# Optimization experiments

Hardware: AMD Instinct MI355X
Metric: run time of the kernel (lower is better)

The kernel has to match this reference:

```python
import jax, jax.numpy as jnp
import numpy as np

N = 2048      # nodes
E = 65536     # edges (avg degree 32)
NV = 6        # n_views (edge_attr dim)
C1, C2, C3 = 32, 32, 32


def _nnconv(x, edge_index, edge_attr, W, b, root, bias, in_c, out_c):
    # Edge MLP: Linear(n_views, in*out) + ReLU -> per-edge weight matrix [E, in, out]
    w = jax.nn.relu(edge_attr @ W + b).reshape(-1, in_c, out_c)
    src, dst = edge_index[0], edge_index[1]  # source_to_target flow
    msg = jnp.einsum('ei,eio->eo', x[src], w)          # gather + edge-specific matmul
    summed = jax.ops.segment_sum(msg, dst, num_segments=N)
    cnt = jax.ops.segment_sum(jnp.ones((msg.shape[0],), x.dtype), dst, num_segments=N)
    agg = summed / jnp.maximum(cnt, 1.0)[:, None]       # scatter-mean (0 for isolated nodes)
    return agg + x @ root + bias                        # root weight + bias (PyG NNConv defaults)


def setup_inputs() -> dict:
    key = jax.random.key(0)
    ks = jax.random.split(key, 12)
    s = 0.1
    return {
        'x': jax.random.normal(ks[0], (N, 1), jnp.float32),
        'edge_attr': jax.random.uniform(ks[1], (E, NV), jnp.float32),
        'edge_index': jax.random.randint(ks[2], (2, E), 0, N, jnp.int64),
        'W1': jax.random.normal(ks[3], (NV, 1 * C1), jnp.float32) * s,
        'b1': jnp.zeros((1 * C1,), jnp.float32),
        'root1': jax.random.normal(ks[4], (1, C1), jnp.float32) * s,
        'bias1': jnp.zeros((C1,), jnp.float32),
        'W2': jax.random.normal(ks[5], (NV, C1 * C2), jnp.float32) * s,
        'b2': jnp.zeros((C1 * C2,), jnp.float32),
        'root2': jax.random.normal(ks[6], (C1, C2), jnp.float32) * s,
        'bias2': jnp.zeros((C2,), jnp.float32),
        'W3': jax.random.normal(ks[7], (NV, C2 * C3), jnp.float32) * s,
        'b3': jnp.zeros((C2 * C3,), jnp.float32),
        'root3': jax.random.normal(ks[8], (C2, C3), jnp.float32) * s,
        'bias3': jnp.zeros((C3,), jnp.float32),
    }


def reference(x, edge_attr, edge_index, W1, b1, root1, bias1, W2, b2, root2, bias2, W3, b3, root3, bias3):
    h = jax.nn.relu(_nnconv(x, edge_index, edge_attr, W1, b1, root1, bias1, 1, C1))
    h = jax.nn.relu(_nnconv(h, edge_index, edge_attr, W2, b2, root2, bias2, C1, C2))
    h = jax.nn.relu(_nnconv(h, edge_index, edge_attr, W3, b3, root3, bias3, C2, C3))
    # CBT: cbt[i, j] = sum_k |h[j, k] - h[i, k]|  (all-pairs L1 distance, [N, N])
    cbt = jnp.sum(jnp.abs(h[None, :, :] - h[:, None, :]), axis=2)
    return cbt
```

## Files before the change

### kernel.cpp

```cpp
#include <hip/hip_runtime.h>

#define N_NODES 2048
#define N_EDGES 65536
#define NV 6
#define C 32


__global__ void edge1_kernel(const float* __restrict__ x,
                             const float* __restrict__ ea,
                             const int* __restrict__ src,
                             const int* __restrict__ dst,
                             const float* __restrict__ W1,
                             const float* __restrict__ b1,
                             float* __restrict__ sum1,
                             float* __restrict__ cnt) {
    int t = blockIdx.x * blockDim.x + threadIdx.x;
    int e = t >> 5, o = t & 31;
    if (e >= N_EDGES) return;
    const float* eap = ea + e * NV;
    float w = b1[o];
#pragma unroll
    for (int v = 0; v < NV; v++) w += eap[v] * W1[v * C + o];
    w = fmaxf(w, 0.0f);
    int d = dst[e];
    atomicAdd(&sum1[d * C + o], x[src[e]] * w);
    if (o == 0) atomicAdd(&cnt[d], 1.0f);
}

template <int IN_C>
__global__ void node_kernel(const float* __restrict__ sum,
                            const float* __restrict__ cnt,
                            const float* __restrict__ hprev,
                            const float* __restrict__ root,
                            const float* __restrict__ bias,
                            float* __restrict__ hout) {
    int t = blockIdx.x * blockDim.x + threadIdx.x;
    int n = t >> 5, o = t & 31;
    float inv = 1.0f / fmaxf(cnt[n], 1.0f);
    float acc = sum[t] * inv + bias[o];
#pragma unroll
    for (int i = 0; i < IN_C; i++) acc += hprev[n * IN_C + i] * root[i * C + o];
    hout[t] = fmaxf(acc, 0.0f);
}

__global__ __launch_bounds__(256) void edge23_kernel(
    const float* __restrict__ hprev,
    const float* __restrict__ ea,
    const int* __restrict__ src,
    const int* __restrict__ dst,
    const float* __restrict__ W,
    const float* __restrict__ b,
    float* __restrict__ sumout)
{
    __shared__ float Wall[7 * 1024];
    __shared__ float hb[4][32 * 4];
    for (int i = threadIdx.x; i < 6 * 1024; i += 256) Wall[i] = W[i];
    for (int i = threadIdx.x; i < 1024; i += 256) Wall[6 * 1024 + i] = b[i];
    __syncthreads();

    const int lane = threadIdx.x & 63;
    const int o = lane & 31;
    const int i0 = (lane >> 5) * 16;
    const int w = threadIdx.x >> 6;
    const int wid = (blockIdx.x * 256 + threadIdx.x) >> 6;
    const int nwaves = (gridDim.x * 256) >> 6;
    float* hbw = &hb[w][0];

    for (int g = wid; g < N_EDGES / 4; g += nwaves) {
        const int e0 = g * 4;
        int s0 = src[e0 + 0], s1 = src[e0 + 1], s2 = src[e0 + 2], s3 = src[e0 + 3];
        int d0 = dst[e0 + 0], d1 = dst[e0 + 1], d2 = dst[e0 + 2], d3 = dst[e0 + 3];
        const float* eap = ea + (size_t)e0 * NV;
        float ea0[NV], ea1[NV], ea2[NV], ea3[NV];
#pragma unroll
        for (int v = 0; v < NV; v++) {
            ea0[v] = eap[v];
            ea1[v] = eap[NV + v];
            ea2[v] = eap[2 * NV + v];
            ea3[v] = eap[3 * NV + v];
        }
        float hv0 = hprev[s0 * C + o];
        float hv1 = hprev[s1 * C + o];
        float hv2 = hprev[s2 * C + o];
        float hv3 = hprev[s3 * C + o];
        __builtin_amdgcn_s_waitcnt(0xc07f);
        if (lane < 32) {
            float4 hq = {hv0, hv1, hv2, hv3};
            *(float4*)&hbw[lane * 4] = hq;
        }
        __builtin_amdgcn_s_waitcnt(0xc07f);

        float acc0 = 0.0f, acc1 = 0.0f, acc2 = 0.0f, acc3 = 0.0f;
#pragma unroll
        for (int j = 0; j < 16; j++) {
            const int idx = (i0 + j) * C + o;
            const float w0 = Wall[0 * 1024 + idx];
            const float w1 = Wall[1 * 1024 + idx];
            const float w2 = Wall[2 * 1024 + idx];
            const float w3 = Wall[3 * 1024 + idx];
            const float w4 = Wall[4 * 1024 + idx];
            const float w5 = Wall[5 * 1024 + idx];
            const float bb = Wall[6 * 1024 + idx];
            const float4 hq = *(const float4*)&hbw[(i0 + j) * 4];
            float t0 = bb + ea0[0] * w0 + ea0[1] * w1 + ea0[2] * w2 + ea0[3] * w3 + ea0[4] * w4 + ea0[5] * w5;
            float t1 = bb + ea1[0] * w0 + ea1[1] * w1 + ea1[2] * w2 + ea1[3] * w3 + ea1[4] * w4 + ea1[5] * w5;
            float t2 = bb + ea2[0] * w0 + ea2[1] * w1 + ea2[2] * w2 + ea2[3] * w3 + ea2[4] * w4 + ea2[5] * w5;
            float t3 = bb + ea3[0] * w0 + ea3[1] * w1 + ea3[2] * w2 + ea3[3] * w3 + ea3[4] * w4 + ea3[5] * w5;
            acc0 += hq.x * fmaxf(t0, 0.0f);
            acc1 += hq.y * fmaxf(t1, 0.0f);
            acc2 += hq.z * fmaxf(t2, 0.0f);
            acc3 += hq.w * fmaxf(t3, 0.0f);
        }
        acc0 += __shfl_down(acc0, 32);
        acc1 += __shfl_down(acc1, 32);
        acc2 += __shfl_down(acc2, 32);
        acc3 += __shfl_down(acc3, 32);
        if (lane < 32) {
            atomicAdd(&sumout[d0 * C + o], acc0);
            atomicAdd(&sumout[d1 * C + o], acc1);
            atomicAdd(&sumout[d2 * C + o], acc2);
            atomicAdd(&sumout[d3 * C + o], acc3);
        }
    }
}

__global__ __launch_bounds__(256) void cbt_kernel(const float* __restrict__ h,
                                                  float* __restrict__ out) {
    __shared__ float hj_s[64][33];
    __shared__ float hi_s[64 * 32];
    const int lane = threadIdx.x & 63;
    const int w = threadIdx.x >> 6;
    const int j0 = blockIdx.x * 64;
    const int i0 = blockIdx.y * 64;
    for (int t = threadIdx.x; t < 64 * 32; t += 256) {
        hj_s[t >> 5][t & 31] = h[j0 * 32 + t];
        hi_s[t] = h[i0 * 32 + t];
    }
    __syncthreads();
    float hj[32];
#pragma unroll
    for (int k = 0; k < 32; k++) hj[k] = hj_s[lane][k];
    const int j = j0 + lane;
#pragma unroll 4
    for (int ii = w * 16; ii < w * 16 + 16; ii++) {
        float acc = 0.0f;
#pragma unroll
        for (int k = 0; k < 32; k++) {
            acc += fabsf(hi_s[ii * 32 + k] - hj[k]);
        }
        out[(size_t)(i0 + ii) * N_NODES + j] = acc;
    }
}

extern "C" void kernel_launch(void* const* d_in, const int* in_sizes, int n_in,
                              void* d_out, int out_size, void* d_ws, size_t ws_size,
                              hipStream_t stream) {
    const float* x         = (const float*)d_in[0];
    const float* edge_attr = (const float*)d_in[1];
    const int*   edge_idx  = (const int*)d_in[2];
    const float* W1 = (const float*)d_in[3];
    const float* b1 = (const float*)d_in[4];
    const float* root1 = (const float*)d_in[5];
    const float* bias1 = (const float*)d_in[6];
    const float* W2 = (const float*)d_in[7];
    const float* b2 = (const float*)d_in[8];
    const float* root2 = (const float*)d_in[9];
    const float* bias2 = (const float*)d_in[10];
    const float* W3 = (const float*)d_in[11];
    const float* b3 = (const float*)d_in[12];
    const float* root3 = (const float*)d_in[13];
    const float* bias3 = (const float*)d_in[14];

    const int* src = edge_idx;
    const int* dst = edge_idx + N_EDGES;

    float* ws   = (float*)d_ws;
    float* cnt  = ws;
    float* sum1 = ws + N_NODES;
    float* sum2 = sum1 + N_NODES * C;
    float* sum3 = sum2 + N_NODES * C;
    float* h1   = sum3 + N_NODES * C;
    float* h2   = h1 + N_NODES * C;
    float* h3   = h2 + N_NODES * C;

    hipMemsetAsync(d_ws, 0, (size_t)(N_NODES + 3 * N_NODES * C) * sizeof(float), stream);

    edge1_kernel<<<(N_EDGES * C) / 256, 256, 0, stream>>>(x, edge_attr, src, dst, W1, b1, sum1, cnt);
    node_kernel<1><<<(N_NODES * C) / 256, 256, 0, stream>>>(sum1, cnt, x, root1, bias1, h1);

    edge23_kernel<<<2048, 256, 0, stream>>>(h1, edge_attr, src, dst, W2, b2, sum2);
    node_kernel<C><<<(N_NODES * C) / 256, 256, 0, stream>>>(sum2, cnt, h1, root2, bias2, h2);

    edge23_kernel<<<2048, 256, 0, stream>>>(h2, edge_attr, src, dst, W3, b3, sum3);
    node_kernel<C><<<(N_NODES * C) / 256, 256, 0, stream>>>(sum3, cnt, h2, root3, bias3, h3);

    cbt_kernel<<<dim3(N_NODES / 64, N_NODES / 64), 256, 0, stream>>>(h3, (float*)d_out);
}
```

Measured before the change: 173.4 us.

## Replace atomic scatter-mean with CSR gather and packed-FP32 edge messages

```diff
diff --git a/kernel.cpp b/kernel.cpp
--- a/kernel.cpp
+++ b/kernel.cpp
@@ -5,55 +5,72 @@
 #define NV 6
 #define C 32
 
+typedef float f2 __attribute__((ext_vector_type(2)));
+
+
+__global__ void hist_kernel(const int* __restrict__ dst, int* __restrict__ cnt) {
+    int e = blockIdx.x * blockDim.x + threadIdx.x;
+    if (e < N_EDGES) atomicAdd(&cnt[dst[e]], 1);
+}
+
+__global__ __launch_bounds__(256) void scan_kernel(const int* __restrict__ cnt,
+                                                   int* __restrict__ rowptr) {
+    __shared__ int part[256];
+    const int tid = threadIdx.x;
+    int local[8];
+    int s = 0;
+#pragma unroll
+    for (int k = 0; k < 8; k++) { local[k] = cnt[tid * 8 + k]; s += local[k]; }
+    part[tid] = s;
+    __syncthreads();
+    for (int off = 1; off < 256; off <<= 1) {
+        int v = (tid >= off) ? part[tid - off] : 0;
+        __syncthreads();
+        part[tid] += v;
+        __syncthreads();
+    }
+    int run = part[tid] - s;
+#pragma unroll
+    for (int k = 0; k < 8; k++) { rowptr[tid * 8 + k] = run; run += local[k]; }
+    if (tid == 255) rowptr[2048] = run;
+}
+
+__global__ void scatter_kernel(const int* __restrict__ dst, const int* __restrict__ rowptr,
+                               int* __restrict__ cursor, int* __restrict__ eid) {
+    int e = blockIdx.x * blockDim.x + threadIdx.x;
+    if (e < N_EDGES) {
+        int d = dst[e];
+        int pos = atomicAdd(&cursor[d], 1);
+        eid[rowptr[d] + pos] = e;
+    }
+}
 
 __global__ void edge1_kernel(const float* __restrict__ x,
                              const float* __restrict__ ea,
                              const int* __restrict__ src,
-                             const int* __restrict__ dst,
                              const float* __restrict__ W1,
                              const float* __restrict__ b1,
-                             float* __restrict__ sum1,
-                             float* __restrict__ cnt) {
+                             float* __restrict__ msg) {
     int t = blockIdx.x * blockDim.x + threadIdx.x;
     int e = t >> 5, o = t & 31;
     if (e >= N_EDGES) return;
     const float* eap = ea + e * NV;
     float w = b1[o];
 #pragma unroll
-    for (int v = 0; v < NV; v++) w += eap[v] * W1[v * C + o];
-    w = fmaxf(w, 0.0f);
-    int d = dst[e];
-    atomicAdd(&sum1[d * C + o], x[src[e]] * w);
-    if (o == 0) atomicAdd(&cnt[d], 1.0f);
-}
-
-template <int IN_C>
-__global__ void node_kernel(const float* __restrict__ sum,
-                            const float* __restrict__ cnt,
-                            const float* __restrict__ hprev,
-                            const float* __restrict__ root,
-                            const float* __restrict__ bias,
-                            float* __restrict__ hout) {
-    int t = blockIdx.x * blockDim.x + threadIdx.x;
-    int n = t >> 5, o = t & 31;
-    float inv = 1.0f / fmaxf(cnt[n], 1.0f);
-    float acc = sum[t] * inv + bias[o];
-#pragma unroll
-    for (int i = 0; i < IN_C; i++) acc += hprev[n * IN_C + i] * root[i * C + o];
-    hout[t] = fmaxf(acc, 0.0f);
+    for (int v = 0; v < NV; v++) w = fmaf(eap[v], W1[v * C + o], w);
+    msg[t] = x[src[e]] * fmaxf(w, 0.0f);
 }
 
 __global__ __launch_bounds__(256) void edge23_kernel(
     const float* __restrict__ hprev,
     const float* __restrict__ ea,
     const int* __restrict__ src,
-    const int* __restrict__ dst,
     const float* __restrict__ W,
     const float* __restrict__ b,
-    float* __restrict__ sumout)
+    float* __restrict__ msg)
 {
     __shared__ float Wall[7 * 1024];
-    __shared__ float hb[4][32 * 4];
+    __shared__ float hb[4][32 * 8];
     for (int i = threadIdx.x; i < 6 * 1024; i += 256) Wall[i] = W[i];
     for (int i = threadIdx.x; i < 1024; i += 256) Wall[6 * 1024 + i] = b[i];
     __syncthreads();
@@ -64,64 +81,100 @@
     const int w = threadIdx.x >> 6;
     const int wid = (blockIdx.x * 256 + threadIdx.x) >> 6;
     const int nwaves = (gridDim.x * 256) >> 6;
+    const int kq = (lane >> 5) << 2;
     float* hbw = &hb[w][0];
 
-    for (int g = wid; g < N_EDGES / 4; g += nwaves) {
-        const int e0 = g * 4;
-        int s0 = src[e0 + 0], s1 = src[e0 + 1], s2 = src[e0 + 2], s3 = src[e0 + 3];
-        int d0 = dst[e0 + 0], d1 = dst[e0 + 1], d2 = dst[e0 + 2], d3 = dst[e0 + 3];
-        const float* eap = ea + (size_t)e0 * NV;
-        float ea0[NV], ea1[NV], ea2[NV], ea3[NV];
-#pragma unroll
-        for (int v = 0; v < NV; v++) {
-            ea0[v] = eap[v];
-            ea1[v] = eap[NV + v];
-            ea2[v] = eap[2 * NV + v];
-            ea3[v] = eap[3 * NV + v];
-        }
-        float hv0 = hprev[s0 * C + o];
-        float hv1 = hprev[s1 * C + o];
-        float hv2 = hprev[s2 * C + o];
-        float hv3 = hprev[s3 * C + o];
-        __builtin_amdgcn_s_waitcnt(0xc07f);
-        if (lane < 32) {
-            float4 hq = {hv0, hv1, hv2, hv3};
-            *(float4*)&hbw[lane * 4] = hq;
-        }
-        __builtin_amdgcn_s_waitcnt(0xc07f);
-
-        float acc0 = 0.0f, acc1 = 0.0f, acc2 = 0.0f, acc3 = 0.0f;
+    for (int g = wid; g < N_EDGES / 8; g += nwaves) {
+        const int e0 = g * 8;
+        const int4 sq = *(const int4*)&src[e0 + kq];
+        union { float4 q[12]; float f[48]; } eau;
+        const float4* eap4 = (const float4*)(ea + (size_t)e0 * NV);
+#pragma unroll
+        for (int t = 0; t < 12; t++) eau.q[t] = eap4[t];
+        float4 hq;
+        hq.x = hprev[sq.x * C + o];
+        hq.y = hprev[sq.y * C + o];
+        hq.z = hprev[sq.z * C + o];
+        hq.w = hprev[sq.w * C + o];
+        *(float4*)&hbw[o * 8 + kq] = hq;
+        f2 p[4][6];
+#pragma unroll
+        for (int a = 0; a < 4; a++)
+#pragma unroll
+            for (int v = 0; v < 6; v++)
+                p[a][v] = (f2){eau.f[a * 12 + v], eau.f[a * 12 + 6 + v]};
+
+        f2 acc[4] = {(f2)(0.0f), (f2)(0.0f), (f2)(0.0f), (f2)(0.0f)};
+        const f2 zero2 = (f2)(0.0f);
 #pragma unroll
         for (int j = 0; j < 16; j++) {
             const int idx = (i0 + j) * C + o;
-            const float w0 = Wall[0 * 1024 + idx];
-            const float w1 = Wall[1 * 1024 + idx];
-            const float w2 = Wall[2 * 1024 + idx];
-            const float w3 = Wall[3 * 1024 + idx];
-            const float w4 = Wall[4 * 1024 + idx];
-            const float w5 = Wall[5 * 1024 + idx];
-            const float bb = Wall[6 * 1024 + idx];
-            const float4 hq = *(const float4*)&hbw[(i0 + j) * 4];
-            float t0 = bb + ea0[0] * w0 + ea0[1] * w1 + ea0[2] * w2 + ea0[3] * w3 + ea0[4] * w4 + ea0[5] * w5;
-            float t1 = bb + ea1[0] * w0 + ea1[1] * w1 + ea1[2] * w2 + ea1[3] * w3 + ea1[4] * w4 + ea1[5] * w5;
-            float t2 = bb + ea2[0] * w0 + ea2[1] * w1 + ea2[2] * w2 + ea2[3] * w3 + ea2[4] * w4 + ea2[5] * w5;
-            float t3 = bb + ea3[0] * w0 + ea3[1] * w1 + ea3[2] * w2 + ea3[3] * w3 + ea3[4] * w4 + ea3[5] * w5;
-            acc0 += hq.x * fmaxf(t0, 0.0f);
-            acc1 += hq.y * fmaxf(t1, 0.0f);
-            acc2 += hq.z * fmaxf(t2, 0.0f);
-            acc3 += hq.w * fmaxf(t3, 0.0f);
+            const float w0 = Wall[idx];
+            const float w1 = Wall[1024 + idx];
+            const float w2 = Wall[2048 + idx];
+            const float w3 = Wall[3072 + idx];
+            const float w4 = Wall[4096 + idx];
+            const float w5 = Wall[5120 + idx];
+            const float bb = Wall[6144 + idx];
+            const float4 h03 = *(const float4*)&hbw[(i0 + j) * 8];
+            const float4 h47 = *(const float4*)&hbw[(i0 + j) * 8 + 4];
+            const f2 hp[4] = {(f2){h03.x, h03.y}, (f2){h03.z, h03.w},
+                              (f2){h47.x, h47.y}, (f2){h47.z, h47.w}};
+            const f2 W0 = (f2)(w0), W1v = (f2)(w1), W2v = (f2)(w2);
+            const f2 W3v = (f2)(w3), W4v = (f2)(w4), W5v = (f2)(w5);
+            const f2 BB = (f2)(bb);
+#pragma unroll
+            for (int a = 0; a < 4; a++) {
+                f2 t = BB;
+                t += p[a][0] * W0;
+                t += p[a][1] * W1v;
+                t += p[a][2] * W2v;
+                t += p[a][3] * W3v;
+                t += p[a][4] * W4v;
+                t += p[a][5] * W5v;
+                t = __builtin_elementwise_max(t, zero2);
+                acc[a] += hp[a] * t;
+            }
         }
-        acc0 += __shfl_down(acc0, 32);
-        acc1 += __shfl_down(acc1, 32);
-        acc2 += __shfl_down(acc2, 32);
-        acc3 += __shfl_down(acc3, 32);
+        float accs[8];
+#pragma unroll
+        for (int a = 0; a < 4; a++) { accs[2 * a] = acc[a].x; accs[2 * a + 1] = acc[a].y; }
+#pragma unroll
+        for (int k = 0; k < 8; k++) accs[k] += __shfl_down(accs[k], 32);
         if (lane < 32) {
-            atomicAdd(&sumout[d0 * C + o], acc0);
-            atomicAdd(&sumout[d1 * C + o], acc1);
-            atomicAdd(&sumout[d2 * C + o], acc2);
-            atomicAdd(&sumout[d3 * C + o], acc3);
+            float* mp = msg + (size_t)e0 * C + o;
+#pragma unroll
+            for (int k = 0; k < 8; k++) mp[k * C] = accs[k];
         }
     }
+}
+
+template <int IN_C>
+__global__ __launch_bounds__(256) void gather_kernel(
+    const float* __restrict__ msg, const int* __restrict__ rowptr,
+    const int* __restrict__ eid, const float* __restrict__ hprev,
+    const float* __restrict__ root,
+    const float* __restrict__ bias,
+    float* __restrict__ hout) {
+    const int o = threadIdx.x & 31;
+    const int n = blockIdx.x * 8 + (threadIdx.x >> 5);
+    const int beg = rowptr[n], end = rowptr[n + 1];
+    float acc = 0.0f;
+    int k = beg;
+    for (; k + 4 <= end; k += 4) {
+        int ka = eid[k], kb = eid[k + 1], kc = eid[k + 2], kd = eid[k + 3];
+        float m0 = msg[ka * C + o];
+        float m1 = msg[kb * C + o];
+        float m2 = msg[kc * C + o];
+        float m3 = msg[kd * C + o];
+        acc += (m0 + m1) + (m2 + m3);
+    }
+    for (; k < end; k++) acc += msg[eid[k] * C + o];
+    const float inv = 1.0f / fmaxf((float)(end - beg), 1.0f);
+    float r = fmaf(acc, inv, bias[o]);
+#pragma unroll
+    for (int i = 0; i < IN_C; i++) r = fmaf(hprev[n * IN_C + i], root[i * C + o], r);
+    hout[n * C + o] = fmaxf(r, 0.0f);
 }
 
 __global__ __launch_bounds__(256) void cbt_kernel(const float* __restrict__ h,
@@ -174,25 +227,30 @@
     const int* src = edge_idx;
     const int* dst = edge_idx + N_EDGES;
 
-    float* ws   = (float*)d_ws;
-    float* cnt  = ws;
-    float* sum1 = ws + N_NODES;
-    float* sum2 = sum1 + N_NODES * C;
-    float* sum3 = sum2 + N_NODES * C;
-    float* h1   = sum3 + N_NODES * C;
+    int* wsi    = (int*)d_ws;
+    int* cnt_i  = wsi;
+    int* cursor = wsi + 2048;
+    int* rowptr = wsi + 4096;
+    int* eid    = wsi + 6160;
+    float* msg  = (float*)(wsi + 6160 + 65536);
+    float* h1   = msg + (size_t)N_EDGES * C;
     float* h2   = h1 + N_NODES * C;
     float* h3   = h2 + N_NODES * C;
 
-    hipMemsetAsync(d_ws, 0, (size_t)(N_NODES + 3 * N_NODES * C) * sizeof(float), stream);
-
-    edge1_kernel<<<(N_EDGES * C) / 256, 256, 0, stream>>>(x, edge_attr, src, dst, W1, b1, sum1, cnt);
-    node_kernel<1><<<(N_NODES * C) / 256, 256, 0, stream>>>(sum1, cnt, x, root1, bias1, h1);
-
-    edge23_kernel<<<2048, 256, 0, stream>>>(h1, edge_attr, src, dst, W2, b2, sum2);
-    node_kernel<C><<<(N_NODES * C) / 256, 256, 0, stream>>>(sum2, cnt, h1, root2, bias2, h2);
-
-    edge23_kernel<<<2048, 256, 0, stream>>>(h2, edge_attr, src, dst, W3, b3, sum3);
-    node_kernel<C><<<(N_NODES * C) / 256, 256, 0, stream>>>(sum3, cnt, h2, root3, bias3, h3);
+    hipMemsetAsync(d_ws, 0, 4096 * sizeof(int), stream);
+
+    hist_kernel<<<N_EDGES / 256, 256, 0, stream>>>(dst, cnt_i);
+    scan_kernel<<<1, 256, 0, stream>>>(cnt_i, rowptr);
+    scatter_kernel<<<N_EDGES / 256, 256, 0, stream>>>(dst, rowptr, cursor, eid);
+
+    edge1_kernel<<<(N_EDGES * C) / 256, 256, 0, stream>>>(x, edge_attr, src, W1, b1, msg);
+    gather_kernel<1><<<N_NODES / 8, 256, 0, stream>>>(msg, rowptr, eid, x, root1, bias1, h1);
+
+    edge23_kernel<<<2048, 256, 0, stream>>>(h1, edge_attr, src, W2, b2, msg);
+    gather_kernel<C><<<N_NODES / 8, 256, 0, stream>>>(msg, rowptr, eid, h1, root2, bias2, h2);
+
+    edge23_kernel<<<2048, 256, 0, stream>>>(h2, edge_attr, src, W3, b3, msg);
+    gather_kernel<C><<<N_NODES / 8, 256, 0, stream>>>(msg, rowptr, eid, h2, root3, bias3, h3);
 
     cbt_kernel<<<dim3(N_NODES / 64, N_NODES / 64), 256, 0, stream>>>(h3, (float*)d_out);
 }
```

Result: slower. 270.2 us (+55.8%).

## Process eight edges per wave in edge kernel with bias kept in registers

Applied to the files above, without the earlier changes.

```diff
diff --git a/kernel.cpp b/kernel.cpp
--- a/kernel.cpp
+++ b/kernel.cpp
@@ -20,7 +20,7 @@
     const float* eap = ea + e * NV;
     float w = b1[o];
 #pragma unroll
-    for (int v = 0; v < NV; v++) w += eap[v] * W1[v * C + o];
+    for (int v = 0; v < NV; v++) w = fmaf(eap[v], W1[v * C + o], w);
     w = fmaxf(w, 0.0f);
     int d = dst[e];
     atomicAdd(&sum1[d * C + o], x[src[e]] * w);
@@ -39,11 +39,11 @@
     float inv = 1.0f / fmaxf(cnt[n], 1.0f);
     float acc = sum[t] * inv + bias[o];
 #pragma unroll
-    for (int i = 0; i < IN_C; i++) acc += hprev[n * IN_C + i] * root[i * C + o];
+    for (int i = 0; i < IN_C; i++) acc = fmaf(hprev[n * IN_C + i], root[i * C + o], acc);
     hout[t] = fmaxf(acc, 0.0f);
 }
 
-__global__ __launch_bounds__(256) void edge23_kernel(
+__global__ __launch_bounds__(256, 4) void edge23_kernel(
     const float* __restrict__ hprev,
     const float* __restrict__ ea,
     const int* __restrict__ src,
@@ -52,75 +52,78 @@
     const float* __restrict__ b,
     float* __restrict__ sumout)
 {
-    __shared__ float Wall[7 * 1024];
-    __shared__ float hb[4][32 * 4];
+    __shared__ float Wall[6 * 1024];
+    __shared__ float hb[4][256];
     for (int i = threadIdx.x; i < 6 * 1024; i += 256) Wall[i] = W[i];
-    for (int i = threadIdx.x; i < 1024; i += 256) Wall[6 * 1024 + i] = b[i];
     __syncthreads();
 
     const int lane = threadIdx.x & 63;
     const int o = lane & 31;
-    const int i0 = (lane >> 5) * 16;
+    const int half = lane >> 5;
+    const int i0 = half * 16;
     const int w = threadIdx.x >> 6;
-    const int wid = (blockIdx.x * 256 + threadIdx.x) >> 6;
-    const int nwaves = (gridDim.x * 256) >> 6;
+    const int g = (blockIdx.x * 256 + threadIdx.x) >> 6;
+    const int e0 = g * 8;
     float* hbw = &hb[w][0];
 
-    for (int g = wid; g < N_EDGES / 4; g += nwaves) {
-        const int e0 = g * 4;
-        int s0 = src[e0 + 0], s1 = src[e0 + 1], s2 = src[e0 + 2], s3 = src[e0 + 3];
-        int d0 = dst[e0 + 0], d1 = dst[e0 + 1], d2 = dst[e0 + 2], d3 = dst[e0 + 3];
-        const float* eap = ea + (size_t)e0 * NV;
-        float ea0[NV], ea1[NV], ea2[NV], ea3[NV];
-#pragma unroll
-        for (int v = 0; v < NV; v++) {
-            ea0[v] = eap[v];
-            ea1[v] = eap[NV + v];
-            ea2[v] = eap[2 * NV + v];
-            ea3[v] = eap[3 * NV + v];
+    float breg[16];
+#pragma unroll
+    for (int j = 0; j < 16; j++) breg[j] = b[(i0 + j) * C + o];
+
+    float eaf[48];
+    const float4* eap4 = (const float4*)(ea + (size_t)e0 * NV);
+#pragma unroll
+    for (int t = 0; t < 12; t++) *(float4*)&eaf[t * 4] = eap4[t];
+
+    const int4 sq = *(const int4*)&src[e0 + half * 4];
+    float4 hq;
+    hq.x = hprev[sq.x * C + o];
+    hq.y = hprev[sq.y * C + o];
+    hq.z = hprev[sq.z * C + o];
+    hq.w = hprev[sq.w * C + o];
+    *(float4*)&hbw[half * 128 + o * 4] = hq;
+
+    float acc[8] = {0, 0, 0, 0, 0, 0, 0, 0};
+#pragma unroll
+    for (int j = 0; j < 16; j++) {
+        const int idx = (i0 + j) * C + o;
+        const float w0 = Wall[idx];
+        const float w1 = Wall[1024 + idx];
+        const float w2 = Wall[2048 + idx];
+        const float w3 = Wall[3072 + idx];
+        const float w4 = Wall[4096 + idx];
+        const float w5 = Wall[5120 + idx];
+        const float bb = breg[j];
+        const float4 hA = *(const float4*)&hbw[(i0 + j) * 4];
+        const float4 hB = *(const float4*)&hbw[128 + (i0 + j) * 4];
+        const float hv[8] = {hA.x, hA.y, hA.z, hA.w, hB.x, hB.y, hB.z, hB.w};
+#pragma unroll
+        for (int k = 0; k < 8; k++) {
+            const float* eap = &eaf[k * 6];
+            float t = bb;
+            t = fmaf(eap[0], w0, t);
+            t = fmaf(eap[1], w1, t);
+            t = fmaf(eap[2], w2, t);
+            t = fmaf(eap[3], w3, t);
+            t = fmaf(eap[4], w4, t);
+            t = fmaf(eap[5], w5, t);
+            acc[k] = fmaf(hv[k], fmaxf(t, 0.0f), acc[k]);
         }
-        float hv0 = hprev[s0 * C + o];
-        float hv1 = hprev[s1 * C + o];
-        float hv2 = hprev[s2 * C + o];
-        float hv3 = hprev[s3 * C + o];
-        __builtin_amdgcn_s_waitcnt(0xc07f);
-        if (lane < 32) {
-            float4 hq = {hv0, hv1, hv2, hv3};
-            *(float4*)&hbw[lane * 4] = hq;
-        }
-        __builtin_amdgcn_s_waitcnt(0xc07f);
-
-        float acc0 = 0.0f, acc1 = 0.0f, acc2 = 0.0f, acc3 = 0.0f;
-#pragma unroll
-        for (int j = 0; j < 16; j++) {
-            const int idx = (i0 + j) * C + o;
-            const float w0 = Wall[0 * 1024 + idx];
-            const float w1 = Wall[1 * 1024 + idx];
-            const float w2 = Wall[2 * 1024 + idx];
-            const float w3 = Wall[3 * 1024 + idx];
-            const float w4 = Wall[4 * 1024 + idx];
-            const float w5 = Wall[5 * 1024 + idx];
-            const float bb = Wall[6 * 1024 + idx];
-            const float4 hq = *(const float4*)&hbw[(i0 + j) * 4];
-            float t0 = bb + ea0[0] * w0 + ea0[1] * w1 + ea0[2] * w2 + ea0[3] * w3 + ea0[4] * w4 + ea0[5] * w5;
-            float t1 = bb + ea1[0] * w0 + ea1[1] * w1 + ea1[2] * w2 + ea1[3] * w3 + ea1[4] * w4 + ea1[5] * w5;
-            float t2 = bb + ea2[0] * w0 + ea2[1] * w1 + ea2[2] * w2 + ea2[3] * w3 + ea2[4] * w4 + ea2[5] * w5;
-            float t3 = bb + ea3[0] * w0 + ea3[1] * w1 + ea3[2] * w2 + ea3[3] * w3 + ea3[4] * w4 + ea3[5] * w5;
-            acc0 += hq.x * fmaxf(t0, 0.0f);
-            acc1 += hq.y * fmaxf(t1, 0.0f);
-            acc2 += hq.z * fmaxf(t2, 0.0f);
-            acc3 += hq.w * fmaxf(t3, 0.0f);
-        }
-        acc0 += __shfl_down(acc0, 32);
-        acc1 += __shfl_down(acc1, 32);
-        acc2 += __shfl_down(acc2, 32);
-        acc3 += __shfl_down(acc3, 32);
-        if (lane < 32) {
-            atomicAdd(&sumout[d0 * C + o], acc0);
-            atomicAdd(&sumout[d1 * C + o], acc1);
-            atomicAdd(&sumout[d2 * C + o], acc2);
-            atomicAdd(&sumout[d3 * C + o], acc3);
-        }
+    }
+#pragma unroll
+    for (int k = 0; k < 8; k++) acc[k] += __shfl_down(acc[k], 32);
+
+    const int4 dA = *(const int4*)&dst[e0];
+    const int4 dB = *(const int4*)&dst[e0 + 4];
+    if (lane < 32) {
+        atomicAdd(&sumout[dA.x * C + o], acc[0]);
+        atomicAdd(&sumout[dA.y * C + o], acc[1]);
+        atomicAdd(&sumout[dA.z * C + o], acc[2]);
+        atomicAdd(&sumout[dA.w * C + o], acc[3]);
+        atomicAdd(&sumout[dB.x * C + o], acc[4]);
+        atomicAdd(&sumout[dB.y * C + o], acc[5]);
+        atomicAdd(&sumout[dB.z * C + o], acc[6]);
+        atomicAdd(&sumout[dB.w * C + o], acc[7]);
     }
 }
 
```

New measurement: 169.4 us. 2.3% less time.
